# Performance work log

Measured on AMD Instinct MI355X. Metric: run time of the kernel, lower is better.

The kernel has to match this reference:

```python
import jax, jax.numpy as jnp
import numpy as np

N_EMBD = 1024
N_HEAD = 16
HEAD_DIM = N_EMBD // N_HEAD


def setup_inputs() -> dict:
    key = jax.random.key(0)
    ks = jax.random.split(key, 9)
    B, T, C = 4, 2048, N_EMBD
    s = 1.0 / np.sqrt(C)
    return {
        "x": jax.random.normal(ks[0], (B, T, C), dtype=jnp.float32),
        "Wq": jax.random.normal(ks[1], (C, C), dtype=jnp.float32) * s,
        "bq": jnp.zeros((C,), dtype=jnp.float32),
        "Wk": jax.random.normal(ks[2], (C, C), dtype=jnp.float32) * s,
        "bk": jnp.zeros((C,), dtype=jnp.float32),
        "Wv": jax.random.normal(ks[3], (C, C), dtype=jnp.float32) * s,
        "bv": jnp.zeros((C,), dtype=jnp.float32),
        "Wo": jax.random.normal(ks[4], (C, C), dtype=jnp.float32) * s,
        "bo": jnp.zeros((C,), dtype=jnp.float32),
    }


def reference(x, Wq, bq, Wk, bk, Wv, bv, Wo, bo):
    B, T, C = x.shape
    H, D = N_HEAD, HEAD_DIM
    # torch Linear: y = x @ W.T + b ; here W stored as (in, out) so y = x @ W + b
    q = (x @ Wq + bq).reshape(B, T, H, D).transpose(0, 2, 1, 3)  # [B,H,T,D]
    k = (x @ Wk + bk).reshape(B, T, H, D).transpose(0, 2, 1, 3)
    v = (x @ Wv + bv).reshape(B, T, H, D).transpose(0, 2, 1, 3)
    scores = jnp.einsum('bhqd,bhkd->bhqk', q, k) / jnp.sqrt(jnp.float32(D))
    causal = jnp.tril(jnp.ones((T, T), dtype=bool))  # [T,T]
    scores = jnp.where(causal[None, None, :, :], scores, -jnp.inf)
    weights = jax.nn.softmax(scores, axis=-1)
    # dropout disabled (eval mode / deterministic reference)
    out = jnp.einsum('bhqk,bhkd->bhqd', weights, v)  # [B,H,T,D]
    out = out.transpose(0, 2, 1, 3).reshape(B, T, C)
    return out @ Wo + bo
```

## Files before the change

kernel.cpp:

```cpp
#include <hip/hip_runtime.h>
#include <stdint.h>
#include <stddef.h>

#define NB 4
#define NT 2048
#define NC 1024
#define NH 16
#define ND 64
#define NM (NB*NT)
#define KVB 64

typedef __bf16 bf16_t;
typedef __attribute__((ext_vector_type(8)))  __bf16 bf16x8;
typedef __attribute__((ext_vector_type(4)))  __bf16 bf16x4;
typedef __attribute__((ext_vector_type(2)))  __bf16 bf16x2;
typedef __attribute__((ext_vector_type(4)))  float  f32x4;
typedef __attribute__((ext_vector_type(16))) float  f32x16;
typedef __attribute__((ext_vector_type(4)))  unsigned int u32x4;

#define QK_SCALE_LOG2E 0.18033688011112042f

__device__ __forceinline__ f32x4 mfma_bf16(bf16x8 a, bf16x8 b, f32x4 c) {
  return __builtin_amdgcn_mfma_f32_16x16x32_bf16(a, b, c, 0, 0, 0);
}
__device__ __forceinline__ f32x16 mfma32(bf16x8 a, bf16x8 b, f32x16 c) {
  return __builtin_amdgcn_mfma_f32_32x32x16_bf16(a, b, c, 0, 0, 0);
}

__device__ __forceinline__ void gld_lds16(const void* g, void* l) {
  __builtin_amdgcn_global_load_lds(
      (const __attribute__((address_space(1))) void*)g,
      (__attribute__((address_space(3))) void*)l, 16, 0, 0);
}

__device__ __forceinline__ unsigned int pack_bf16(float a, float b) {
  bf16x2 t; t[0] = (bf16_t)a; t[1] = (bf16_t)b;
  return __builtin_bit_cast(unsigned int, t);
}

#if __has_builtin(__builtin_amdgcn_permlane32_swap)
typedef __attribute__((ext_vector_type(2))) unsigned int u32x2;
__device__ __forceinline__ void plswap(unsigned int &a, unsigned int &b) {
  u32x2 r = __builtin_amdgcn_permlane32_swap(a, b, false, false);
  a = r[0]; b = r[1];
}
#else
__device__ __forceinline__ void plswap(unsigned int &a, unsigned int &b) {
  asm volatile("s_nop 1\n\tv_permlane32_swap_b32 %0, %1\n\ts_nop 1"
               : "+v"(a), "+v"(b));
}
#endif

__global__ __launch_bounds__(256) void cast_x_kernel(const float* __restrict__ x,
                                                     bf16_t* __restrict__ xb, int n4) {
  const int stride = gridDim.x * blockDim.x;
  for (int i = blockIdx.x * blockDim.x + threadIdx.x; i < n4; i += stride) {
    float4 v = reinterpret_cast<const float4*>(x)[i];
    bf16x4 o;
    o[0] = (bf16_t)v.x; o[1] = (bf16_t)v.y; o[2] = (bf16_t)v.z; o[3] = (bf16_t)v.w;
    reinterpret_cast<bf16x4*>(xb)[i] = o;
  }
}

__global__ __launch_bounds__(256) void transpose_cast_kernel(const float* __restrict__ W,
                                                             bf16_t* __restrict__ WT) {
  __shared__ float tile[32][33];
  const int t = threadIdx.x;
  const int tx = t & 31, ty = t >> 5;
  const int k0 = (blockIdx.x & 31) << 5;
  const int n0 = (blockIdx.x >> 5) << 5;
#pragma unroll
  for (int i = 0; i < 4; ++i)
    tile[ty + 8*i][tx] = W[(size_t)(k0 + ty + 8*i)*NC + n0 + tx];
  __syncthreads();
#pragma unroll
  for (int i = 0; i < 4; ++i)
    WT[(size_t)(n0 + ty + 8*i)*NC + k0 + tx] = (bf16_t)tile[tx][ty + 8*i];
}

template<int MODE>
__global__ __launch_bounds__(256) void gemm_bt_kernel(
    const bf16_t* __restrict__ A, const bf16_t* __restrict__ BT,
    int M, int N, int K,
    bf16_t* __restrict__ qo, bf16_t* __restrict__ ko, bf16_t* __restrict__ vo,
    const float* __restrict__ b0, const float* __restrict__ b1, const float* __restrict__ b2,
    float* __restrict__ outp, const float* __restrict__ bo)
{
  const int lane = threadIdx.x & 63;
  const int wv = threadIdx.x >> 6;
  const int wr = wv >> 1, wc = wv & 1;
  const int l15 = lane & 15, lg = lane >> 4;
  const int nbn = N >> 7;
  const int bm = blockIdx.x / nbn, bn = blockIdx.x % nbn;
  const int m0 = bm << 7, n0 = bn << 7;

  __shared__ char smem[32768];
  char* As = smem;
  char* Bs = smem + 16384;

  f32x4 acc[4][4] = {};

  const int nkt = K >> 6;
  for (int kt = 0; kt < nkt; ++kt) {
    const int k0 = kt << 6;
    __syncthreads();
#pragma unroll
    for (int i = 0; i < 4; ++i) {
      const int seg = i*4 + wv;
      const int lin = seg*64 + lane;
      const int row = lin >> 3;
      const int ch  = (lin & 7) ^ (row & 7);
      gld_lds16(A  + (size_t)(m0 + row)*K + k0 + (ch << 3), As + seg*1024);
      gld_lds16(BT + (size_t)(n0 + row)*K + k0 + (ch << 3), Bs + seg*1024);
    }
    __syncthreads();
#pragma unroll
    for (int ks = 0; ks < 2; ++ks) {
      bf16x8 af[4], bfr[4];
#pragma unroll
      for (int fr = 0; fr < 4; ++fr) {
        const int row = wr*64 + fr*16 + l15;
        const int ch  = (ks*4 + lg) ^ (row & 7);
        af[fr] = *reinterpret_cast<const bf16x8*>(As + row*128 + ch*16);
      }
#pragma unroll
      for (int fc = 0; fc < 4; ++fc) {
        const int row = wc*64 + fc*16 + l15;
        const int ch  = (ks*4 + lg) ^ (row & 7);
        bfr[fc] = *reinterpret_cast<const bf16x8*>(Bs + row*128 + ch*16);
      }
#pragma unroll
      for (int fr = 0; fr < 4; ++fr)
#pragma unroll
        for (int fc = 0; fc < 4; ++fc)
          acc[fr][fc] = mfma_bf16(af[fr], bfr[fc], acc[fr][fc]);
    }
  }

#pragma unroll
  for (int fr = 0; fr < 4; ++fr) {
#pragma unroll
    for (int fc = 0; fc < 4; ++fc) {
      const int mrow0 = m0 + wr*64 + fr*16 + (lg << 2);
      const int ncol  = n0 + wc*64 + fc*16 + l15;
      if (MODE == 0) {
        const int mat = ncol >> 10, c = ncol & 1023;
        const int h = c >> 6, d = c & 63;
        if (mat == 2) {
          const float bias = b2[c];
          bf16x4 ov;
#pragma unroll
          for (int r = 0; r < 4; ++r) ov[r] = (bf16_t)(acc[fr][fc][r] + bias);
          const int bb = mrow0 >> 11, tt = mrow0 & (NT - 1);
          *reinterpret_cast<bf16x4*>(vo + ((((size_t)bb*NH + h)*ND + d)*NT) + tt) = ov;
        } else {
          bf16_t* dst = (mat == 0) ? qo : ko;
          const float* bptr = (mat == 0) ? b0 : b1;
          const float bias = bptr[c];
          const float scl = (mat == 0) ? QK_SCALE_LOG2E : 1.0f;
#pragma unroll
          for (int r = 0; r < 4; ++r) {
            const int mm = mrow0 + r;
            const int bb = mm >> 11, tt = mm & (NT - 1);
            dst[((((size_t)bb*NH + h)*NT + tt) << 6) + d] =
                (bf16_t)((acc[fr][fc][r] + bias) * scl);
          }
        }
      } else {
        const float bias = bo[ncol];
#pragma unroll
        for (int r = 0; r < 4; ++r)
          outp[(size_t)(mrow0 + r)*N + ncol] = acc[fr][fc][r] + bias;
      }
    }
  }
}

__global__ __launch_bounds__(128) void attn_kernel(
    const bf16_t* __restrict__ q, const bf16_t* __restrict__ k, const bf16_t* __restrict__ vt,
    bf16_t* __restrict__ o)
{
  const int tid  = threadIdx.x;
  const int lane = tid & 63;
  const int wv   = tid >> 6;
  const int l31  = lane & 31, h = lane >> 5;

  const int tile = 31 - (blockIdx.x >> 6);
  const int bh   = blockIdx.x & 63;
  const int bb = bh >> 4, hh = bh & 15;
  const int q0 = tile << 6;

  __shared__ char smem[4*8192];
  char* const ks0 = smem;
  char* const ks1 = smem + 8192;
  char* const vs0 = smem + 16384;
  char* const vs1 = smem + 24576;

  const size_t base = (size_t)bh * (NT * ND);
  const bf16_t* Kg = k  + base;
  const bf16_t* Vg = vt + base;

  const int q0w = q0 + wv*32;
  const int qg  = q0w + l31;

  int offk[4], offv[4], segb[4];
#pragma unroll
  for (int p = 0; p < 4; ++p) {
    const int c   = p*128 + tid;
    const int row = c >> 3;
    const int ch  = (c & 7) ^ (row & 7);
    offk[p] = row*ND + (ch << 3);
    offv[p] = row*NT + (ch << 3);
    segb[p] = (p*2 + wv) * 1024;
  }

#pragma unroll
  for (int p = 0; p < 4; ++p) {
    gld_lds16(Kg + offk[p], ks0 + segb[p]);
    gld_lds16(Vg + offv[p], vs0 + segb[p]);
  }

  bf16x8 qf[4];
  {
    const bf16_t* Qg = q + base + (size_t)qg*ND + 8*h;
#pragma unroll
    for (int ds = 0; ds < 4; ++ds)
      qf[ds] = *reinterpret_cast<const bf16x8*>(Qg + 16*ds);
  }

  bf16x8 ones8;
#pragma unroll
  for (int jj = 0; jj < 8; ++jj) ones8[jj] = (bf16_t)1.0f;

  f32x16 oc[2] = {};
  f32x16 lacc = {};

  const int nkv = tile + 1;

  for (int j = 0; j < nkv; ++j) {
    const bool cur1 = (j & 1) != 0;
    char* const Kc = cur1 ? ks1 : ks0;
    char* const Vc = cur1 ? vs1 : vs0;

    asm volatile("s_waitcnt vmcnt(0)" ::: "memory");
    __builtin_amdgcn_s_barrier();
    __builtin_amdgcn_sched_barrier(0);

    if (j + 1 < nkv) {
      char* const Kn = cur1 ? ks0 : ks1;
      char* const Vn = cur1 ? vs0 : vs1;
      const int kadv = (j + 1) * (KVB * ND);
      const int vadv = (j + 1) * KVB;
#pragma unroll
      for (int p = 0; p < 4; ++p) {
        gld_lds16(Kg + kadv + offk[p], Kn + segb[p]);
        gld_lds16(Vg + vadv + offv[p], Vn + segb[p]);
      }
      __builtin_amdgcn_sched_barrier(0);
    }

    f32x16 st[2] = {};
    __builtin_amdgcn_s_setprio(1);
#pragma unroll
    for (int ds = 0; ds < 4; ++ds) {
#pragma unroll
      for (int kt = 0; kt < 2; ++kt) {
        const int row = kt*32 + l31;
        const int cl  = (2*ds + h) ^ (row & 7);
        const bf16x8 kfr = *reinterpret_cast<const bf16x8*>(Kc + row*128 + cl*16);
        st[kt] = mfma32(kfr, qf[ds], st[kt]);
      }
    }
    __builtin_amdgcn_s_setprio(0);

    if (j == nkv - 1) {
      const int qrel = qg - (j << 6) - 4*h;
#pragma unroll
      for (int kt = 0; kt < 2; ++kt)
#pragma unroll
        for (int r = 0; r < 16; ++r) {
          const int kc = (r & 3) + 8*(r >> 2) + 32*kt;
          st[kt][r] = (kc > qrel) ? 0.0f : exp2f(st[kt][r]);
        }
    } else {
#pragma unroll
      for (int kt = 0; kt < 2; ++kt)
#pragma unroll
        for (int r = 0; r < 16; ++r)
          st[kt][r] = exp2f(st[kt][r]);
    }

#pragma unroll
    for (int kt = 0; kt < 2; ++kt) {
#pragma unroll
      for (int g = 0; g < 2; ++g) {
        unsigned int wa = pack_bf16(st[kt][8*g + 0], st[kt][8*g + 1]);
        unsigned int wb = pack_bf16(st[kt][8*g + 2], st[kt][8*g + 3]);
        unsigned int wc = pack_bf16(st[kt][8*g + 4], st[kt][8*g + 5]);
        unsigned int wd = pack_bf16(st[kt][8*g + 6], st[kt][8*g + 7]);
        plswap(wa, wc);
        plswap(wb, wd);
        u32x4 pb; pb[0] = wa; pb[1] = wb; pb[2] = wc; pb[3] = wd;
        const bf16x8 pf = __builtin_bit_cast(bf16x8, pb);
        const int kg = 2*kt + g;
        __builtin_amdgcn_s_setprio(1);
        lacc = mfma32(ones8, pf, lacc);
#pragma unroll
        for (int da = 0; da < 2; ++da) {
          const int row = 32*da + l31;
          const int cl  = (2*kg + h) ^ (row & 7);
          const bf16x8 vf = *reinterpret_cast<const bf16x8*>(Vc + row*128 + cl*16);
          oc[da] = mfma32(vf, pf, oc[da]);
        }
        __builtin_amdgcn_s_setprio(0);
      }
    }
  }

  const float rl = 1.0f / lacc[0];
  bf16_t* orow = o + ((size_t)bb*NT + qg)*NC + hh*ND;
#pragma unroll
  for (int da = 0; da < 2; ++da) {
#pragma unroll
    for (int u = 0; u < 4; ++u) {
      bf16x4 ov;
#pragma unroll
      for (int jj = 0; jj < 4; ++jj) ov[jj] = (bf16_t)(oc[da][4*u + jj] * rl);
      *reinterpret_cast<bf16x4*>(orow + 32*da + 8*u + 4*h) = ov;
    }
  }
}

extern "C" void kernel_launch(void* const* d_in, const int* in_sizes, int n_in,
                              void* d_out, int out_size, void* d_ws, size_t ws_size,
                              hipStream_t stream) {
  (void)in_sizes; (void)n_in; (void)out_size;
  const float* x  = (const float*)d_in[0];
  const float* Wq = (const float*)d_in[1];
  const float* bq = (const float*)d_in[2];
  const float* Wk = (const float*)d_in[3];
  const float* bk = (const float*)d_in[4];
  const float* Wv = (const float*)d_in[5];
  const float* bv = (const float*)d_in[6];
  const float* Wo = (const float*)d_in[7];
  const float* bo = (const float*)d_in[8];
  float* out = (float*)d_out;

  const size_t off_xb    = 0;
  const size_t off_wqkvT = 16777216;
  const size_t off_woT   = 23068672;
  const size_t off_q     = 25165824;
  const size_t off_k     = 41943040;
  const size_t off_v     = 58720256;
  const size_t off_attn  = 75497472;
  const size_t need      = 92274688;
  if (ws_size < need) return;

  char* ws = (char*)d_ws;
  bf16_t* xb    = (bf16_t*)(ws + off_xb);
  bf16_t* wqkvT = (bf16_t*)(ws + off_wqkvT);
  bf16_t* woT   = (bf16_t*)(ws + off_woT);
  bf16_t* qb    = (bf16_t*)(ws + off_q);
  bf16_t* kb    = (bf16_t*)(ws + off_k);
  bf16_t* vtb   = (bf16_t*)(ws + off_v);
  bf16_t* attnb = (bf16_t*)(ws + off_attn);

  cast_x_kernel<<<dim3(2048), dim3(256), 0, stream>>>(x, xb, NM*NC/4);
  transpose_cast_kernel<<<dim3(1024), dim3(256), 0, stream>>>(Wq, wqkvT);
  transpose_cast_kernel<<<dim3(1024), dim3(256), 0, stream>>>(Wk, wqkvT + 1048576);
  transpose_cast_kernel<<<dim3(1024), dim3(256), 0, stream>>>(Wv, wqkvT + 2097152);
  transpose_cast_kernel<<<dim3(1024), dim3(256), 0, stream>>>(Wo, woT);

  gemm_bt_kernel<0><<<dim3(64*24), dim3(256), 0, stream>>>(
      xb, wqkvT, NM, 3*NC, NC, qb, kb, vtb, bq, bk, bv, nullptr, nullptr);

  attn_kernel<<<dim3(32*64), dim3(128), 0, stream>>>(qb, kb, vtb, attnb);

  gemm_bt_kernel<1><<<dim3(64*8), dim3(256), 0, stream>>>(
      attnb, woT, NM, NC, NC, nullptr, nullptr, nullptr, nullptr, nullptr, nullptr,
      out, bo);
}
```

Baseline: 191.4 us.

## Enlarge attention query tile to 256 rows with 8 waves sharing KV tiles

The attention kernel now processes 256 query rows per block using 8 waves (512 threads) instead of 64 rows with 2 waves, so each K/V tile staged in LDS is reused by four times as many queries. Each thread loads one chunk per tile, and waves skip KV tiles entirely above their causal diagonal, masking only tiles that straddle it. This cuts global K/V traffic per query, at the cost of a grid of 512 blocks, which may underfill the GPU, and causal load imbalance across waves in a block that must still hit every barrier.

```diff
diff --git a/kernel.cpp b/kernel.cpp
--- a/kernel.cpp
+++ b/kernel.cpp
@@ -176,7 +176,7 @@
   }
 }
 
-__global__ __launch_bounds__(128) void attn_kernel(
+__global__ __launch_bounds__(512, 4) void attn_kernel(
     const bf16_t* __restrict__ q, const bf16_t* __restrict__ k, const bf16_t* __restrict__ vt,
     bf16_t* __restrict__ o)
 {
@@ -185,10 +185,10 @@
   const int wv   = tid >> 6;
   const int l31  = lane & 31, h = lane >> 5;
 
-  const int tile = 31 - (blockIdx.x >> 6);
+  const int tile = 7 - (blockIdx.x >> 6);
   const int bh   = blockIdx.x & 63;
   const int bb = bh >> 4, hh = bh & 15;
-  const int q0 = tile << 6;
+  const int q0 = tile << 8;
 
   __shared__ char smem[4*8192];
   char* const ks0 = smem;
@@ -203,22 +203,14 @@
   const int q0w = q0 + wv*32;
   const int qg  = q0w + l31;
 
-  int offk[4], offv[4], segb[4];
-#pragma unroll
-  for (int p = 0; p < 4; ++p) {
-    const int c   = p*128 + tid;
-    const int row = c >> 3;
-    const int ch  = (c & 7) ^ (row & 7);
-    offk[p] = row*ND + (ch << 3);
-    offv[p] = row*NT + (ch << 3);
-    segb[p] = (p*2 + wv) * 1024;
-  }
-
-#pragma unroll
-  for (int p = 0; p < 4; ++p) {
-    gld_lds16(Kg + offk[p], ks0 + segb[p]);
-    gld_lds16(Vg + offv[p], vs0 + segb[p]);
-  }
+  const int srow = tid >> 3;
+  const int sch  = (tid & 7) ^ (srow & 7);
+  const int offk = srow*ND + (sch << 3);
+  const int offv = srow*NT + (sch << 3);
+  const int segb = wv << 10;
+
+  gld_lds16(Kg + offk, ks0 + segb);
+  gld_lds16(Vg + offv, vs0 + segb);
 
   bf16x8 qf[4];
   {
@@ -235,9 +227,10 @@
   f32x16 oc[2] = {};
   f32x16 lacc = {};
 
-  const int nkv = tile + 1;
+  const int nkv = 4*(tile + 1);
 
   for (int j = 0; j < nkv; ++j) {
+    const int kt0 = j << 6;
     const bool cur1 = (j & 1) != 0;
     char* const Kc = cur1 ? ks1 : ks0;
     char* const Vc = cur1 ? vs1 : vs0;
@@ -249,70 +242,67 @@
     if (j + 1 < nkv) {
       char* const Kn = cur1 ? ks0 : ks1;
       char* const Vn = cur1 ? vs0 : vs1;
-      const int kadv = (j + 1) * (KVB * ND);
-      const int vadv = (j + 1) * KVB;
-#pragma unroll
-      for (int p = 0; p < 4; ++p) {
-        gld_lds16(Kg + kadv + offk[p], Kn + segb[p]);
-        gld_lds16(Vg + vadv + offv[p], Vn + segb[p]);
-      }
+      gld_lds16(Kg + (j + 1)*(KVB*ND) + offk, Kn + segb);
+      gld_lds16(Vg + (j + 1)*KVB      + offv, Vn + segb);
       __builtin_amdgcn_sched_barrier(0);
     }
 
-    f32x16 st[2] = {};
-    __builtin_amdgcn_s_setprio(1);
-#pragma unroll
-    for (int ds = 0; ds < 4; ++ds) {
+    if (kt0 <= q0w + 31) {
+      f32x16 st[2] = {};
+      __builtin_amdgcn_s_setprio(1);
+#pragma unroll
+      for (int ds = 0; ds < 4; ++ds) {
+#pragma unroll
+        for (int kt = 0; kt < 2; ++kt) {
+          const int row = kt*32 + l31;
+          const int cl  = (2*ds + h) ^ (row & 7);
+          const bf16x8 kfr = *reinterpret_cast<const bf16x8*>(Kc + row*128 + cl*16);
+          st[kt] = mfma32(kfr, qf[ds], st[kt]);
+        }
+      }
+      __builtin_amdgcn_s_setprio(0);
+
+      if (kt0 + KVB - 1 > q0w) {
+        const int qrel = qg - kt0 - 4*h;
+#pragma unroll
+        for (int kt = 0; kt < 2; ++kt)
+#pragma unroll
+          for (int r = 0; r < 16; ++r) {
+            const int kc = (r & 3) + 8*(r >> 2) + 32*kt;
+            st[kt][r] = (kc > qrel) ? 0.0f : exp2f(st[kt][r]);
+          }
+      } else {
+#pragma unroll
+        for (int kt = 0; kt < 2; ++kt)
+#pragma unroll
+          for (int r = 0; r < 16; ++r)
+            st[kt][r] = exp2f(st[kt][r]);
+      }
+
 #pragma unroll
       for (int kt = 0; kt < 2; ++kt) {
-        const int row = kt*32 + l31;
-        const int cl  = (2*ds + h) ^ (row & 7);
-        const bf16x8 kfr = *reinterpret_cast<const bf16x8*>(Kc + row*128 + cl*16);
-        st[kt] = mfma32(kfr, qf[ds], st[kt]);
-      }
-    }
-    __builtin_amdgcn_s_setprio(0);
-
-    if (j == nkv - 1) {
-      const int qrel = qg - (j << 6) - 4*h;
-#pragma unroll
-      for (int kt = 0; kt < 2; ++kt)
-#pragma unroll
-        for (int r = 0; r < 16; ++r) {
-          const int kc = (r & 3) + 8*(r >> 2) + 32*kt;
-          st[kt][r] = (kc > qrel) ? 0.0f : exp2f(st[kt][r]);
+#pragma unroll
+        for (int g = 0; g < 2; ++g) {
+          unsigned int wa = pack_bf16(st[kt][8*g + 0], st[kt][8*g + 1]);
+          unsigned int wb = pack_bf16(st[kt][8*g + 2], st[kt][8*g + 3]);
+          unsigned int wc = pack_bf16(st[kt][8*g + 4], st[kt][8*g + 5]);
+          unsigned int wd = pack_bf16(st[kt][8*g + 6], st[kt][8*g + 7]);
+          plswap(wa, wc);
+          plswap(wb, wd);
+          u32x4 pb; pb[0] = wa; pb[1] = wb; pb[2] = wc; pb[3] = wd;
+          const bf16x8 pf = __builtin_bit_cast(bf16x8, pb);
+          const int kg = 2*kt + g;
+          __builtin_amdgcn_s_setprio(1);
+          lacc = mfma32(ones8, pf, lacc);
+#pragma unroll
+          for (int da = 0; da < 2; ++da) {
+            const int row = 32*da + l31;
+            const int cl  = (2*kg + h) ^ (row & 7);
+            const bf16x8 vf = *reinterpret_cast<const bf16x8*>(Vc + row*128 + cl*16);
+            oc[da] = mfma32(vf, pf, oc[da]);
+          }
+          __builtin_amdgcn_s_setprio(0);
         }
-    } else {
-#pragma unroll
-      for (int kt = 0; kt < 2; ++kt)
-#pragma unroll
-        for (int r = 0; r < 16; ++r)
-          st[kt][r] = exp2f(st[kt][r]);
-    }
-
-#pragma unroll
-    for (int kt = 0; kt < 2; ++kt) {
-#pragma unroll
-      for (int g = 0; g < 2; ++g) {
-        unsigned int wa = pack_bf16(st[kt][8*g + 0], st[kt][8*g + 1]);
-        unsigned int wb = pack_bf16(st[kt][8*g + 2], st[kt][8*g + 3]);
-        unsigned int wc = pack_bf16(st[kt][8*g + 4], st[kt][8*g + 5]);
-        unsigned int wd = pack_bf16(st[kt][8*g + 6], st[kt][8*g + 7]);
-        plswap(wa, wc);
-        plswap(wb, wd);
-        u32x4 pb; pb[0] = wa; pb[1] = wb; pb[2] = wc; pb[3] = wd;
-        const bf16x8 pf = __builtin_bit_cast(bf16x8, pb);
-        const int kg = 2*kt + g;
-        __builtin_amdgcn_s_setprio(1);
-        lacc = mfma32(ones8, pf, lacc);
-#pragma unroll
-        for (int da = 0; da < 2; ++da) {
-          const int row = 32*da + l31;
-          const int cl  = (2*kg + h) ^ (row & 7);
-          const bf16x8 vf = *reinterpret_cast<const bf16x8*>(Vc + row*128 + cl*16);
-          oc[da] = mfma32(vf, pf, oc[da]);
-        }
-        __builtin_amdgcn_s_setprio(0);
       }
     }
   }
@@ -374,7 +364,7 @@
   gemm_bt_kernel<0><<<dim3(64*24), dim3(256), 0, stream>>>(
       xb, wqkvT, NM, 3*NC, NC, qb, kb, vtb, bq, bk, bv, nullptr, nullptr);
 
-  attn_kernel<<<dim3(32*64), dim3(128), 0, stream>>>(qb, kb, vtb, attnb);
+  attn_kernel<<<dim3(8*64), dim3(512), 0, stream>>>(qb, kb, vtb, attnb);
 
   gemm_bt_kernel<1><<<dim3(64*8), dim3(256), 0, stream>>>(
       attnb, woT, NM, NC, NC, nullptr, nullptr, nullptr, nullptr, nullptr, nullptr,
```

Result: slower. 208.8 us (+9.1%).
